# Kernel optimization log

Hardware: AMD Instinct MI355X
Metric: run time of the kernel (lower is better)

## Reference

```python
import jax, jax.numpy as jnp
import numpy as np

D_MODEL = 1024
N_HEADS = 16
HEAD_DIM = D_MODEL // N_HEADS
NUM_MEM = 32
D_FF = 4 * D_MODEL
EPS = 1e-5


def _layer_norm(x, g, b):
    mu = jnp.mean(x, axis=-1, keepdims=True)
    var = jnp.mean(jnp.square(x - mu), axis=-1, keepdims=True)
    return (x - mu) * jax.lax.rsqrt(var + EPS) * g + b


def setup_inputs() -> dict:
    key = jax.random.key(0)
    ks = jax.random.split(key, 16)
    E, F, M = D_MODEL, D_FF, NUM_MEM
    s = 1.0 / np.sqrt(E)
    inp = {
        "src": jax.random.normal(ks[0], (2048, 2, E), dtype=jnp.float32),
        "in_proj_w": jax.random.uniform(ks[1], (3 * E, E), jnp.float32, -s, s),
        "in_proj_b": jnp.zeros((3 * E,), jnp.float32),
        "out_w": jax.random.uniform(ks[2], (E, E), jnp.float32, -s, s),
        "out_b": jnp.zeros((E,), jnp.float32),
        "mem_k": jax.random.normal(ks[3], (M, 1, E), jnp.float32) * (1.0 / HEAD_DIM),
        "mem_v": jax.random.normal(ks[4], (M, 1, E), jnp.float32) * (1.0 / M),
        "w1": jax.random.uniform(ks[5], (F, E), jnp.float32, -s, s),
        "b1": jnp.zeros((F,), jnp.float32),
        "w2": jax.random.uniform(ks[6], (E, F), jnp.float32, -1.0 / np.sqrt(F), 1.0 / np.sqrt(F)),
        "b2": jnp.zeros((E,), jnp.float32),
        "ln1_g": jnp.ones((E,), jnp.float32),
        "ln1_b": jnp.zeros((E,), jnp.float32),
        "ln2_g": jnp.ones((E,), jnp.float32),
        "ln2_b": jnp.zeros((E,), jnp.float32),
    }
    return inp


def reference(src, in_proj_w, in_proj_b, out_w, out_b, mem_k, mem_v,
              w1, b1, w2, b2, ln1_g, ln1_b, ln2_g, ln2_b):
    T, B, E = src.shape
    H, d, M = N_HEADS, HEAD_DIM, NUM_MEM

    # --- self-attention with learned memory k/v tokens (dropout=0, eval) ---
    qkv = src @ in_proj_w.T + in_proj_b          # [T, B, 3E]
    q, k, v = jnp.split(qkv, 3, axis=-1)
    q = q * (d ** -0.5)

    # scaled memory tokens appended to K/V along the sequence axis
    mk = (d ** 0.5) * jnp.broadcast_to(mem_k, (M, B, E))
    mv = (M ** 0.5) * jnp.broadcast_to(mem_v, (M, B, E))
    k = jnp.concatenate([k, mk], axis=0)          # [T+M, B, E]
    v = jnp.concatenate([v, mv], axis=0)

    qh = q.reshape(T, B, H, d)
    kh = k.reshape(T + M, B, H, d)
    vh = v.reshape(T + M, B, H, d)

    scores = jnp.einsum('tbhd,sbhd->bhts', qh, kh)  # [B, H, T, T+M]
    attn = jax.nn.softmax(scores, axis=-1)
    ctx = jnp.einsum('bhts,sbhd->tbhd', attn, vh).reshape(T, B, E)
    attn_out = ctx @ out_w.T + out_b

    # --- residual + LN, FFN, residual + LN (post-norm, relu) ---
    x = _layer_norm(src + attn_out, ln1_g, ln1_b)
    ffn = jax.nn.relu(x @ w1.T + b1) @ w2.T + b2
    return _layer_norm(x + ffn, ln2_g, ln2_b)
```

## Files before the change

### kernel.cpp

```cpp
#include <hip/hip_runtime.h>
#include <hip/hip_bf16.h>
#include <cstdint>


using bf16 = __hip_bfloat16;
typedef __attribute__((ext_vector_type(8))) __bf16 bf16x8;
typedef __attribute__((ext_vector_type(4))) float f32x4;

__device__ __forceinline__ void gload_lds16(const void* g, void* l) {
    auto gp = (const __attribute__((address_space(1))) void*)(uintptr_t)g;
    auto lp = (__attribute__((address_space(3))) void*)(uint32_t)(uintptr_t)l;
    __builtin_amdgcn_global_load_lds(gp, lp, 16, 0, 0);
}

__device__ __forceinline__ float fast_exp2(float x) {
#if __has_builtin(__builtin_amdgcn_exp2f)
    return __builtin_amdgcn_exp2f(x);
#else
    float r;
    asm("v_exp_f32 %0, %1" : "=v"(r) : "v"(x));
    return r;
#endif
}

__device__ __forceinline__ bf16 bf16_rn(float x) {
    uint32_t u = __builtin_bit_cast(uint32_t, x);
    uint16_t h = (uint16_t)((u + 0x8000u) >> 16);
    return __builtin_bit_cast(bf16, h);
}

template <int EPI>
__global__ __launch_bounds__(256, 2) void gemm_bt(
    const bf16* __restrict__ A, const bf16* __restrict__ B,
    const float* __restrict__ bias, const float* __restrict__ res,
    float* __restrict__ Cf, bf16* __restrict__ Cb, int M, int N, int K) {
    __shared__ alignas(16) bf16 As[128 * 32];
    __shared__ alignas(16) bf16 Bs[128 * 32];

    const int tid = threadIdx.x;
    const int wid = tid >> 6;
    const int lane = tid & 63;
    const int g = lane >> 4;
    const int li = lane & 15;

    int wg = blockIdx.y * gridDim.x + blockIdx.x;
    const int nwg = gridDim.x * gridDim.y;
    const int cpx = nwg >> 3;
    wg = (wg & 7) * cpx + (wg >> 3);
    const int bx = wg % (int)gridDim.x;
    const int by = wg / (int)gridDim.x;

    const int row0 = by * 128;
    const int col0 = bx * 128;
    const int wr = (wid >> 1) * 64;
    const int wc = (wid & 1) * 64;

    const int c0 = wid, c1 = wid + 4;
    const int srow = lane >> 2;
    const int scol = (lane & 3) * 8;

    const bf16* Ag0 = A + (size_t)(row0 + c0 * 16 + srow) * K + scol;
    const bf16* Ag1 = A + (size_t)(row0 + c1 * 16 + srow) * K + scol;
    const bf16* Bg0 = B + (size_t)(col0 + c0 * 16 + srow) * K + scol;
    const bf16* Bg1 = B + (size_t)(col0 + c1 * 16 + srow) * K + scol;

    bf16* lA0 = &As[c0 * 512];
    bf16* lA1 = &As[c1 * 512];
    bf16* lB0 = &Bs[c0 * 512];
    bf16* lB1 = &Bs[c1 * 512];

    f32x4 acc[4][4];
#pragma unroll
    for (int i = 0; i < 4; ++i)
#pragma unroll
        for (int j = 0; j < 4; ++j) acc[i][j] = (f32x4){0.f, 0.f, 0.f, 0.f};

    for (int k0 = 0; k0 < K; k0 += 32) {
        gload_lds16(Ag0 + k0, lA0);
        gload_lds16(Ag1 + k0, lA1);
        gload_lds16(Bg0 + k0, lB0);
        gload_lds16(Bg1 + k0, lB1);
        __syncthreads();

        bf16x8 af[4], bfr[4];
#pragma unroll
        for (int i = 0; i < 4; ++i) {
            af[i] = *(const bf16x8*)&As[(wr + i * 16 + li) * 32 + g * 8];
            bfr[i] = *(const bf16x8*)&Bs[(wc + i * 16 + li) * 32 + g * 8];
        }
#pragma unroll
        for (int i = 0; i < 4; ++i)
#pragma unroll
            for (int j = 0; j < 4; ++j)
                acc[i][j] = __builtin_amdgcn_mfma_f32_16x16x32_bf16(af[i], bfr[j], acc[i][j], 0, 0, 0);
        __syncthreads();
    }

#pragma unroll
    for (int i = 0; i < 4; ++i) {
#pragma unroll
        for (int j = 0; j < 4; ++j) {
            const int col = col0 + wc + j * 16 + li;
            const float bv = bias[col];
#pragma unroll
            for (int r = 0; r < 4; ++r) {
                const int row = row0 + wr + i * 16 + g * 4 + r;
                const size_t idx = (size_t)row * N + col;
                float v = acc[i][j][r] + bv;
                if (EPI == 0) {
                    if (col < 1024) v *= 0.18033688011112042f;
                    Cb[idx] = bf16_rn(v);
                } else if (EPI == 1) {
                    Cf[idx] = v + res[idx];
                } else {
                    Cb[idx] = bf16_rn(v > 0.f ? v : 0.f);
                }
            }
        }
    }
}

__global__ __launch_bounds__(256) void transpose_v(const bf16* __restrict__ qkv,
                                                   const bf16* __restrict__ mv,
                                                   bf16* __restrict__ vt) {
    __shared__ bf16 tile[64][72];
    const int t = blockIdx.x;
    const int h = blockIdx.y;
    const int b = blockIdx.z;
    const int tid = threadIdx.x;
    const int r = tid >> 2;
    const int c = (tid & 3) * 16;
    const int s0 = t * 64;
    if (t < 32) {
        const bf16* p = qkv + (size_t)((s0 + r) * 2 + b) * 3072 + 2048 + h * 64 + c;
        *(bf16x8*)&tile[r][c] = *(const bf16x8*)p;
        *(bf16x8*)&tile[r][c + 8] = *(const bf16x8*)(p + 8);
    } else if (r < 32) {
        const bf16* p = mv + (size_t)r * 1024 + h * 64 + c;
        *(bf16x8*)&tile[r][c] = *(const bf16x8*)p;
        *(bf16x8*)&tile[r][c + 8] = *(const bf16x8*)(p + 8);
    }
    __syncthreads();
    const int d = tid >> 2;
    const int sc = (tid & 3) * 16;
    const int smax = (t < 32) ? 64 : 32;
    if (sc < smax) {
        bf16 tmp[16];
#pragma unroll
        for (int j = 0; j < 16; ++j) tmp[j] = tile[sc + j][d];
        bf16* q = vt + (size_t)((b * 16 + h) * 64 + d) * 2080 + s0 + sc;
        *(bf16x8*)q = *(const bf16x8*)&tmp[0];
        *(bf16x8*)(q + 8) = *(const bf16x8*)&tmp[8];
    }
}

__global__ __launch_bounds__(256, 2) void attn_kernel(
    const bf16* __restrict__ qkv, const bf16* __restrict__ mk,
    const bf16* __restrict__ vt, bf16* __restrict__ ctx) {
    __shared__ alignas(16) bf16 Kst[2][64 * 64];
    __shared__ alignas(16) bf16 Vst[2][64 * 64];
    __shared__ alignas(16) bf16 Plds[4][32 * 64];

    const int tid = threadIdx.x;
    const int wid = tid >> 6;
    const int lane = tid & 63;
    const int g = lane >> 4;
    const int li = lane & 15;

    const int h = blockIdx.x;
    const int b = blockIdx.z;
    const int q0 = blockIdx.y * 128 + wid * 32;

    bf16* pl = &Plds[wid][0];
    const bf16* vth = vt + (size_t)((b * 16 + h) * 64) * 2080;

    const int srow8 = lane >> 3;
    const int sslot = (lane & 7) ^ srow8;

#define STAGE_KV(buf, t)                                                                       \
    {                                                                                          \
        const int _s0 = (t) * 64;                                                              \
        _Pragma("unroll") for (int j = 0; j < 2; ++j) {                                        \
            const int rw = (wid * 2 + j) * 8 + srow8;                                          \
            gload_lds16(qkv + (size_t)((_s0 + rw) * 2 + b) * 3072 + 1024 + h * 64 + sslot * 8, \
                        &Kst[buf][(wid * 2 + j) * 512]);                                       \
            gload_lds16(vth + (size_t)rw * 2080 + _s0 + sslot * 8,                             \
                        &Vst[buf][(wid * 2 + j) * 512]);                                       \
        }                                                                                      \
    }

    bf16x8 qf[2][2];
#pragma unroll
    for (int mi = 0; mi < 2; ++mi)
#pragma unroll
        for (int kd = 0; kd < 2; ++kd)
            qf[mi][kd] = *(const bf16x8*)(qkv + (size_t)((q0 + mi * 16 + li) * 2 + b) * 3072 +
                                          h * 64 + kd * 32 + g * 8);

    f32x4 o[2][4];
    float lrow[2][4];
#pragma unroll
    for (int mi = 0; mi < 2; ++mi) {
#pragma unroll
        for (int ni = 0; ni < 4; ++ni) o[mi][ni] = (f32x4){0.f, 0.f, 0.f, 0.f};
#pragma unroll
        for (int r = 0; r < 4; ++r) lrow[mi][r] = 0.f;
    }

    STAGE_KV(0, 0);

    for (int t = 0; t < 32; ++t) {
        const int cur = t & 1;
        __syncthreads();
        if (t < 31) STAGE_KV(cur ^ 1, t + 1);

        bf16x8 kf[4][2];
#pragma unroll
        for (int si = 0; si < 4; ++si)
#pragma unroll
            for (int kd = 0; kd < 2; ++kd)
                kf[si][kd] = *(const bf16x8*)&Kst[cur][(si * 16 + li) * 64 +
                                                       (((kd * 4 + g) ^ (li & 7)) * 8)];

        f32x4 sa[2][4];
#pragma unroll
        for (int mi = 0; mi < 2; ++mi)
#pragma unroll
            for (int si = 0; si < 4; ++si) sa[mi][si] = (f32x4){0.f, 0.f, 0.f, 0.f};
#pragma unroll
        for (int mi = 0; mi < 2; ++mi)
#pragma unroll
            for (int si = 0; si < 4; ++si)
#pragma unroll
                for (int kd = 0; kd < 2; ++kd)
                    sa[mi][si] = __builtin_amdgcn_mfma_f32_16x16x32_bf16(qf[mi][kd], kf[si][kd],
                                                                         sa[mi][si], 0, 0, 0);

        bf16x8 vf[2][4];
#pragma unroll
        for (int sblk = 0; sblk < 2; ++sblk)
#pragma unroll
            for (int ni = 0; ni < 4; ++ni)
                vf[sblk][ni] = *(const bf16x8*)&Vst[cur][(ni * 16 + li) * 64 +
                                                         (((sblk * 4 + g) ^ (li & 7)) * 8)];

#pragma unroll
        for (int mi = 0; mi < 2; ++mi)
#pragma unroll
            for (int r = 0; r < 4; ++r) {
                float ps = 0.f;
#pragma unroll
                for (int si = 0; si < 4; ++si) {
                    const float p = fast_exp2(sa[mi][si][r]);
                    sa[mi][si][r] = p;
                    ps += p;
                }
                lrow[mi][r] += ps;
            }

#pragma unroll
        for (int mi = 0; mi < 2; ++mi)
#pragma unroll
            for (int si = 0; si < 4; ++si)
#pragma unroll
                for (int r = 0; r < 4; ++r) {
                    const int row = mi * 16 + g * 4 + r;
                    const int col = (si * 16 + li) ^ (((row >> 2) & 3) << 4);
                    pl[row * 64 + col] = bf16_rn(sa[mi][si][r]);
                }

        asm volatile("s_waitcnt lgkmcnt(0)" ::: "memory");
        __builtin_amdgcn_sched_barrier(0);

        bf16x8 pa[2][2];
#pragma unroll
        for (int mi = 0; mi < 2; ++mi)
#pragma unroll
            for (int sblk = 0; sblk < 2; ++sblk) {
                const int row = mi * 16 + li;
                const int e = (sblk * 32 + g * 8) ^ (((row >> 2) & 3) << 4);
                pa[mi][sblk] = *(const bf16x8*)&pl[row * 64 + e];
            }

#pragma unroll
        for (int sblk = 0; sblk < 2; ++sblk)
#pragma unroll
            for (int ni = 0; ni < 4; ++ni)
#pragma unroll
                for (int mi = 0; mi < 2; ++mi)
                    o[mi][ni] = __builtin_amdgcn_mfma_f32_16x16x32_bf16(pa[mi][sblk], vf[sblk][ni],
                                                                        o[mi][ni], 0, 0, 0);
    }

    {
        bf16x8 kf[2][2];
#pragma unroll
        for (int si = 0; si < 2; ++si)
#pragma unroll
            for (int kd = 0; kd < 2; ++kd)
                kf[si][kd] = *(const bf16x8*)(mk + (size_t)(si * 16 + li) * 1024 + h * 64 +
                                              kd * 32 + g * 8);
        bf16x8 vf[4];
#pragma unroll
        for (int ni = 0; ni < 4; ++ni)
            vf[ni] = *(const bf16x8*)(vth + (size_t)(ni * 16 + li) * 2080 + 2048 + g * 8);

        f32x4 sa[2][2];
#pragma unroll
        for (int mi = 0; mi < 2; ++mi)
#pragma unroll
            for (int si = 0; si < 2; ++si) sa[mi][si] = (f32x4){0.f, 0.f, 0.f, 0.f};
#pragma unroll
        for (int mi = 0; mi < 2; ++mi)
#pragma unroll
            for (int si = 0; si < 2; ++si)
#pragma unroll
                for (int kd = 0; kd < 2; ++kd)
                    sa[mi][si] = __builtin_amdgcn_mfma_f32_16x16x32_bf16(qf[mi][kd], kf[si][kd],
                                                                         sa[mi][si], 0, 0, 0);
#pragma unroll
        for (int mi = 0; mi < 2; ++mi)
#pragma unroll
            for (int r = 0; r < 4; ++r) {
                float ps = 0.f;
#pragma unroll
                for (int si = 0; si < 2; ++si) {
                    const float p = fast_exp2(sa[mi][si][r]);
                    sa[mi][si][r] = p;
                    ps += p;
                }
                lrow[mi][r] += ps;
            }
#pragma unroll
        for (int mi = 0; mi < 2; ++mi)
#pragma unroll
            for (int si = 0; si < 2; ++si)
#pragma unroll
                for (int r = 0; r < 4; ++r) {
                    const int row = mi * 16 + g * 4 + r;
                    const int col = (si * 16 + li) ^ (((row >> 2) & 3) << 4);
                    pl[row * 64 + col] = bf16_rn(sa[mi][si][r]);
                }

        asm volatile("s_waitcnt lgkmcnt(0)" ::: "memory");
        __builtin_amdgcn_sched_barrier(0);

        bf16x8 pa[2];
#pragma unroll
        for (int mi = 0; mi < 2; ++mi) {
            const int row = mi * 16 + li;
            const int e = (g * 8) ^ (((row >> 2) & 3) << 4);
            pa[mi] = *(const bf16x8*)&pl[row * 64 + e];
        }
#pragma unroll
        for (int ni = 0; ni < 4; ++ni)
#pragma unroll
            for (int mi = 0; mi < 2; ++mi)
                o[mi][ni] = __builtin_amdgcn_mfma_f32_16x16x32_bf16(pa[mi], vf[ni], o[mi][ni], 0, 0, 0);
    }

#pragma unroll
    for (int mi = 0; mi < 2; ++mi)
#pragma unroll
        for (int r = 0; r < 4; ++r) {
            float s = lrow[mi][r];
#pragma unroll
            for (int d = 1; d < 16; d <<= 1) s += __shfl_xor(s, d);
            const float inv = 1.f / s;
            const int trow = q0 + mi * 16 + g * 4 + r;
#pragma unroll
            for (int ni = 0; ni < 4; ++ni)
                ctx[(size_t)(trow * 2 + b) * 1024 + h * 64 + ni * 16 + li] =
                    bf16_rn(o[mi][ni][r] * inv);
        }
#undef STAGE_KV
}

__global__ __launch_bounds__(256, 4) void ln_kernel(
    const float* __restrict__ x, const float* __restrict__ gw,
    const float* __restrict__ bw, float* __restrict__ y, bf16* __restrict__ ybf) {
    const int row = blockIdx.x;
    const int tid = threadIdx.x;
    const float4 v = ((const float4*)(x + (size_t)row * 1024))[tid];
    float s = v.x + v.y + v.z + v.w;
    float s2 = v.x * v.x + v.y * v.y + v.z * v.z + v.w * v.w;
#pragma unroll
    for (int d = 1; d < 64; d <<= 1) {
        s += __shfl_xor(s, d);
        s2 += __shfl_xor(s2, d);
    }
    __shared__ float red[8];
    const int wid = tid >> 6, lane = tid & 63;
    if (lane == 0) { red[wid] = s; red[4 + wid] = s2; }
    __syncthreads();
    s = red[0] + red[1] + red[2] + red[3];
    s2 = red[4] + red[5] + red[6] + red[7];
    const float mu = s * (1.f / 1024.f);
    const float var = s2 * (1.f / 1024.f) - mu * mu;
    const float rstd = rsqrtf(var + 1e-5f);
    const float4 gv = ((const float4*)gw)[tid];
    const float4 bv = ((const float4*)bw)[tid];
    float4 out;
    out.x = (v.x - mu) * rstd * gv.x + bv.x;
    out.y = (v.y - mu) * rstd * gv.y + bv.y;
    out.z = (v.z - mu) * rstd * gv.z + bv.z;
    out.w = (v.w - mu) * rstd * gv.w + bv.w;
    ((float4*)(y + (size_t)row * 1024))[tid] = out;
    if (ybf) {
        bf16* yb = ybf + (size_t)row * 1024 + tid * 4;
        yb[0] = bf16_rn(out.x);
        yb[1] = bf16_rn(out.y);
        yb[2] = bf16_rn(out.z);
        yb[3] = bf16_rn(out.w);
    }
}

__global__ void cvt_kernel(const float* __restrict__ in, bf16* __restrict__ out, float scale,
                           int n4) {
    const int i = blockIdx.x * 256 + threadIdx.x;
    if (i >= n4) return;
    const float4 v = ((const float4*)in)[i];
    bf16* op = out + (size_t)i * 4;
    op[0] = bf16_rn(v.x * scale);
    op[1] = bf16_rn(v.y * scale);
    op[2] = bf16_rn(v.z * scale);
    op[3] = bf16_rn(v.w * scale);
}

extern "C" void kernel_launch(void* const* d_in, const int* in_sizes, int n_in, void* d_out,
                              int out_size, void* d_ws, size_t ws_size, hipStream_t stream) {
    const float* src = (const float*)d_in[0];
    const float* inproj_w = (const float*)d_in[1];
    const float* inproj_b = (const float*)d_in[2];
    const float* outw = (const float*)d_in[3];
    const float* outb = (const float*)d_in[4];
    const float* memk = (const float*)d_in[5];
    const float* memv = (const float*)d_in[6];
    const float* w1 = (const float*)d_in[7];
    const float* b1 = (const float*)d_in[8];
    const float* w2 = (const float*)d_in[9];
    const float* b2 = (const float*)d_in[10];
    const float* ln1g = (const float*)d_in[11];
    const float* ln1b = (const float*)d_in[12];
    const float* ln2g = (const float*)d_in[13];
    const float* ln2b = (const float*)d_in[14];

    char* ws = (char*)d_ws;
    const size_t MB = 1024 * 1024;
    bf16* w_inproj_bf = (bf16*)(ws + 0);
    bf16* w_out_bf = (bf16*)(ws + 6 * MB);
    bf16* w1_bf = (bf16*)(ws + 8 * MB);
    bf16* w2_bf = (bf16*)(ws + 16 * MB);
    bf16* mk_bf = (bf16*)(ws + 24 * MB);
    bf16* mv_bf = (bf16*)(ws + 24 * MB + 65536);
    bf16* src_bf = (bf16*)(ws + 25 * MB);
    bf16* ctx_bf = src_bf;
    bf16* qkv_bf = (bf16*)(ws + 33 * MB);
    bf16* h_bf = qkv_bf;
    float* pre1 = (float*)(ws + 65 * MB);
    bf16* vt_bf = (bf16*)(ws + 65 * MB);
    float* pre2 = pre1;
    float* x_f = (float*)(ws + 81 * MB);
    bf16* x_bf = (bf16*)(ws + 97 * MB);
    float* outp = (float*)d_out;

    auto cvt = [&](const float* in, bf16* out, float scale, int n) {
        int n4 = n / 4;
        cvt_kernel<<<dim3((n4 + 255) / 256), dim3(256), 0, stream>>>(in, out, scale, n4);
    };
    cvt(src, src_bf, 1.f, 4096 * 1024);
    cvt(inproj_w, w_inproj_bf, 1.f, 3072 * 1024);
    cvt(outw, w_out_bf, 1.f, 1024 * 1024);
    cvt(w1, w1_bf, 1.f, 4096 * 1024);
    cvt(w2, w2_bf, 1.f, 4096 * 1024);
    cvt(memk, mk_bf, 8.f, 32 * 1024);
    cvt(memv, mv_bf, 5.656854249492381f, 32 * 1024);

    gemm_bt<0><<<dim3(3072 / 128, 4096 / 128), 256, 0, stream>>>(
        src_bf, w_inproj_bf, inproj_b, nullptr, nullptr, qkv_bf, 4096, 3072, 1024);
    transpose_v<<<dim3(33, 16, 2), 256, 0, stream>>>(qkv_bf, mv_bf, vt_bf);
    attn_kernel<<<dim3(16, 16, 2), 256, 0, stream>>>(qkv_bf, mk_bf, vt_bf, ctx_bf);
    gemm_bt<1><<<dim3(1024 / 128, 4096 / 128), 256, 0, stream>>>(
        ctx_bf, w_out_bf, outb, src, pre1, nullptr, 4096, 1024, 1024);
    ln_kernel<<<dim3(4096), 256, 0, stream>>>(pre1, ln1g, ln1b, x_f, x_bf);
    gemm_bt<2><<<dim3(4096 / 128, 4096 / 128), 256, 0, stream>>>(
        x_bf, w1_bf, b1, nullptr, nullptr, h_bf, 4096, 4096, 1024);
    gemm_bt<1><<<dim3(1024 / 128, 4096 / 128), 256, 0, stream>>>(
        h_bf, w2_bf, b2, x_f, pre2, nullptr, 4096, 1024, 4096);
    ln_kernel<<<dim3(4096), 256, 0, stream>>>(pre2, ln2g, ln2b, outp, nullptr);
}
```

Measured before the change: 276.9 us.

## Split-K the N=1024 GEMMs and fuse partial sum plus residual into LayerNorm

The out-projection and FFN-down GEMMs become split-K=2 launches via blockIdx.z, doubling the workgroup count from 256 to 512. This is meant to fill the GPU better, since those grids previously covered only half the resident-block capacity. Each split writes a bf16 partial, and the LayerNorm kernel now sums the two partials with the fp32 residual, replacing the fp32 pre-LN buffer writes. The trade-off is extra rounding from storing partials in bf16, plus a second partial buffer to read.

```diff
diff --git a/kernel.cpp b/kernel.cpp
--- a/kernel.cpp
+++ b/kernel.cpp
@@ -5,6 +5,7 @@
 
 using bf16 = __hip_bfloat16;
 typedef __attribute__((ext_vector_type(8))) __bf16 bf16x8;
+typedef __attribute__((ext_vector_type(4))) __bf16 bf16x4;
 typedef __attribute__((ext_vector_type(4))) float f32x4;
 
 __device__ __forceinline__ void gload_lds16(const void* g, void* l) {
@@ -29,11 +30,15 @@
     return __builtin_bit_cast(bf16, h);
 }
 
+__device__ __forceinline__ float bf2f(__bf16 x) {
+    return (float)x;
+}
+
 template <int EPI>
 __global__ __launch_bounds__(256, 2) void gemm_bt(
     const bf16* __restrict__ A, const bf16* __restrict__ B,
-    const float* __restrict__ bias, const float* __restrict__ res,
-    float* __restrict__ Cf, bf16* __restrict__ Cb, int M, int N, int K) {
+    const float* __restrict__ bias, bf16* __restrict__ Cb,
+    int M, int N, int K, int lda) {
     __shared__ alignas(16) bf16 As[128 * 32];
     __shared__ alignas(16) bf16 Bs[128 * 32];
 
@@ -42,6 +47,12 @@
     const int lane = tid & 63;
     const int g = lane >> 4;
     const int li = lane & 15;
+
+    if (EPI == 3) {
+        const int zo = blockIdx.z * K;
+        A += zo;
+        B += zo;
+    }
 
     int wg = blockIdx.y * gridDim.x + blockIdx.x;
     const int nwg = gridDim.x * gridDim.y;
@@ -59,10 +70,10 @@
     const int srow = lane >> 2;
     const int scol = (lane & 3) * 8;
 
-    const bf16* Ag0 = A + (size_t)(row0 + c0 * 16 + srow) * K + scol;
-    const bf16* Ag1 = A + (size_t)(row0 + c1 * 16 + srow) * K + scol;
-    const bf16* Bg0 = B + (size_t)(col0 + c0 * 16 + srow) * K + scol;
-    const bf16* Bg1 = B + (size_t)(col0 + c1 * 16 + srow) * K + scol;
+    const bf16* Ag0 = A + (size_t)(row0 + c0 * 16 + srow) * lda + scol;
+    const bf16* Ag1 = A + (size_t)(row0 + c1 * 16 + srow) * lda + scol;
+    const bf16* Bg0 = B + (size_t)(col0 + c0 * 16 + srow) * lda + scol;
+    const bf16* Bg1 = B + (size_t)(col0 + c1 * 16 + srow) * lda + scol;
 
     bf16* lA0 = &As[c0 * 512];
     bf16* lA1 = &As[c1 * 512];
@@ -101,7 +112,7 @@
 #pragma unroll
         for (int j = 0; j < 4; ++j) {
             const int col = col0 + wc + j * 16 + li;
-            const float bv = bias[col];
+            const float bv = (EPI == 3 && blockIdx.z != 0) ? 0.f : bias[col];
 #pragma unroll
             for (int r = 0; r < 4; ++r) {
                 const int row = row0 + wr + i * 16 + g * 4 + r;
@@ -110,10 +121,10 @@
                 if (EPI == 0) {
                     if (col < 1024) v *= 0.18033688011112042f;
                     Cb[idx] = bf16_rn(v);
-                } else if (EPI == 1) {
-                    Cf[idx] = v + res[idx];
+                } else if (EPI == 2) {
+                    Cb[idx] = bf16_rn(v > 0.f ? v : 0.f);
                 } else {
-                    Cb[idx] = bf16_rn(v > 0.f ? v : 0.f);
+                    Cb[(size_t)blockIdx.z * ((size_t)M * N) + idx] = bf16_rn(v);
                 }
             }
         }
@@ -376,12 +387,22 @@
 #undef STAGE_KV
 }
 
-__global__ __launch_bounds__(256, 4) void ln_kernel(
-    const float* __restrict__ x, const float* __restrict__ gw,
-    const float* __restrict__ bw, float* __restrict__ y, bf16* __restrict__ ybf) {
+__global__ __launch_bounds__(256, 4) void ln_sum_kernel(
+    const bf16* __restrict__ p0, const bf16* __restrict__ p1, const float* __restrict__ xres,
+    const float* __restrict__ gw, const float* __restrict__ bw,
+    float* __restrict__ y, bf16* __restrict__ ybf) {
     const int row = blockIdx.x;
     const int tid = threadIdx.x;
-    const float4 v = ((const float4*)(x + (size_t)row * 1024))[tid];
+    const size_t base = (size_t)row * 1024 + tid * 4;
+    const bf16x4 a0 = *(const bf16x4*)(p0 + base);
+    const bf16x4 a1 = *(const bf16x4*)(p1 + base);
+    const float4 xr = ((const float4*)(xres + (size_t)row * 1024))[tid];
+    float4 v;
+    v.x = bf2f(a0[0]) + bf2f(a1[0]) + xr.x;
+    v.y = bf2f(a0[1]) + bf2f(a1[1]) + xr.y;
+    v.z = bf2f(a0[2]) + bf2f(a1[2]) + xr.z;
+    v.w = bf2f(a0[3]) + bf2f(a1[3]) + xr.w;
+
     float s = v.x + v.y + v.z + v.w;
     float s2 = v.x * v.x + v.y * v.y + v.z * v.z + v.w * v.w;
 #pragma unroll
@@ -405,9 +426,9 @@
     out.y = (v.y - mu) * rstd * gv.y + bv.y;
     out.z = (v.z - mu) * rstd * gv.z + bv.z;
     out.w = (v.w - mu) * rstd * gv.w + bv.w;
-    ((float4*)(y + (size_t)row * 1024))[tid] = out;
+    if (y) ((float4*)(y + (size_t)row * 1024))[tid] = out;
     if (ybf) {
-        bf16* yb = ybf + (size_t)row * 1024 + tid * 4;
+        bf16* yb = ybf + base;
         yb[0] = bf16_rn(out.x);
         yb[1] = bf16_rn(out.y);
         yb[2] = bf16_rn(out.z);
@@ -455,11 +476,12 @@
     bf16* mv_bf = (bf16*)(ws + 24 * MB + 65536);
     bf16* src_bf = (bf16*)(ws + 25 * MB);
     bf16* ctx_bf = src_bf;
+    bf16* g4p = src_bf;
     bf16* qkv_bf = (bf16*)(ws + 33 * MB);
     bf16* h_bf = qkv_bf;
-    float* pre1 = (float*)(ws + 65 * MB);
     bf16* vt_bf = (bf16*)(ws + 65 * MB);
-    float* pre2 = pre1;
+    bf16* g2p = vt_bf;
+    bf16* g4p1 = vt_bf;
     float* x_f = (float*)(ws + 81 * MB);
     bf16* x_bf = (bf16*)(ws + 97 * MB);
     float* outp = (float*)d_out;
@@ -477,15 +499,17 @@
     cvt(memv, mv_bf, 5.656854249492381f, 32 * 1024);
 
     gemm_bt<0><<<dim3(3072 / 128, 4096 / 128), 256, 0, stream>>>(
-        src_bf, w_inproj_bf, inproj_b, nullptr, nullptr, qkv_bf, 4096, 3072, 1024);
+        src_bf, w_inproj_bf, inproj_b, qkv_bf, 4096, 3072, 1024, 1024);
     transpose_v<<<dim3(33, 16, 2), 256, 0, stream>>>(qkv_bf, mv_bf, vt_bf);
     attn_kernel<<<dim3(16, 16, 2), 256, 0, stream>>>(qkv_bf, mk_bf, vt_bf, ctx_bf);
-    gemm_bt<1><<<dim3(1024 / 128, 4096 / 128), 256, 0, stream>>>(
-        ctx_bf, w_out_bf, outb, src, pre1, nullptr, 4096, 1024, 1024);
-    ln_kernel<<<dim3(4096), 256, 0, stream>>>(pre1, ln1g, ln1b, x_f, x_bf);
+    gemm_bt<3><<<dim3(1024 / 128, 4096 / 128, 2), 256, 0, stream>>>(
+        ctx_bf, w_out_bf, outb, g2p, 4096, 1024, 512, 1024);
+    ln_sum_kernel<<<dim3(4096), 256, 0, stream>>>(g2p, g2p + (size_t)4096 * 1024, src, ln1g, ln1b,
+                                                  x_f, x_bf);
     gemm_bt<2><<<dim3(4096 / 128, 4096 / 128), 256, 0, stream>>>(
-        x_bf, w1_bf, b1, nullptr, nullptr, h_bf, 4096, 4096, 1024);
-    gemm_bt<1><<<dim3(1024 / 128, 4096 / 128), 256, 0, stream>>>(
-        h_bf, w2_bf, b2, x_f, pre2, nullptr, 4096, 1024, 4096);
-    ln_kernel<<<dim3(4096), 256, 0, stream>>>(pre2, ln2g, ln2b, outp, nullptr);
-}
+        x_bf, w1_bf, b1, h_bf, 4096, 4096, 1024, 1024);
+    gemm_bt<3><<<dim3(1024 / 128, 4096 / 128, 2), 256, 0, stream>>>(
+        h_bf, w2_bf, b2, g2p, 4096, 1024, 2048, 4096);
+    ln_sum_kernel<<<dim3(4096), 256, 0, stream>>>(g2p, g2p + (size_t)4096 * 1024, x_f, ln2g, ln2b,
+                                                  outp, nullptr);
+}
```

Measured after the change: 247.5 us. 1.12x faster.
